# Optimization experiments

Measured on AMD Instinct MI355X. Metric: run time of the kernel, lower is better.

The kernel has to match this reference:

```python
import jax, jax.numpy as jnp
import numpy as np

DIM = 4096
RATIO = 0.5
K = max(1, int(np.ceil(RATIO * DIM)))  # 2048


def setup_inputs() -> dict:
    key = jax.random.key(0)
    x = jax.random.normal(key, (4, 4096, DIM), dtype=jnp.float32)
    return {"x": x}


def reference(x):
    # Eval-mode exact path of TopKSiLU with _thr == 0:
    #   h = silu(x); thr = kth largest |h| per row; zero entries with |h| < thr.
    h = jax.nn.silu(x)
    abs_h = jnp.abs(h)
    # torch kthvalue(dim - k + 1) over ascending order == k-th largest value.
    topk_vals, _ = jax.lax.top_k(abs_h, K)          # [..., K], descending
    thr = topk_vals[..., -1:]                        # [..., 1] per-row threshold
    return jnp.where(abs_h < thr, jnp.zeros((), x.dtype), h)
```

## Files before the change

kernel.cpp:

```cpp
#include <hip/hip_runtime.h>
#include <math.h>

#define DIM      4096
#define KSEL     2048
#define NTHREADS 256
#define VPT      16
#define NREP     8
#define HSTRIDE  257
#define HREP_SZ  (NREP * HSTRIDE)

__device__ __forceinline__ float cephes_expf_fma(float x) {
    const float LOG2EF = 1.44269504088896341f;
    const float C1     = 0.693359375f;
    const float C2     = -2.12194440e-4f;
    float z0 = __builtin_fmaf(x, LOG2EF, 0.5f);
    float fx = floorf(z0);
    float r  = __fsub_rn(x, __fmul_rn(fx, C1));
    r = __builtin_fmaf(fx, -C2, r);
    float zz = __fmul_rn(r, r);
    float y  = 1.9875691500e-4f;
    y = __builtin_fmaf(y, r, 1.3981999507e-3f);
    y = __builtin_fmaf(y, r, 8.3334519073e-3f);
    y = __builtin_fmaf(y, r, 4.1665795894e-2f);
    y = __builtin_fmaf(y, r, 1.6666665459e-1f);
    y = __builtin_fmaf(y, r, 5.0000001201e-1f);
    y = __builtin_fmaf(y, zz, r);
    y = __fadd_rn(y, 1.0f);
    int n = (int)fx;
    float scale = __int_as_float((n + 127) << 23);
    return __fmul_rn(y, scale);
}

__device__ __forceinline__ float silu_ref(float x) {
    float e = cephes_expf_fma(-x);
    float s = __fdiv_rn(1.0f, __fadd_rn(1.0f, e));
    return __fmul_rn(x, s);
}

__global__ __launch_bounds__(NTHREADS) void topk_silu_kernel(
    const float* __restrict__ x, float* __restrict__ out)
{
    const int row  = blockIdx.x;
    const int tid  = threadIdx.x;
    const int lane = tid & 63;
    const int wave = tid >> 6;

    const float4* __restrict__ xr4 =
        reinterpret_cast<const float4*>(x + (size_t)row * DIM);
    float4* __restrict__ or4 =
        reinterpret_cast<float4*>(out + (size_t)row * DIM);

    __shared__ int      hrep[HREP_SZ];
    __shared__ int      hist1[256];
    __shared__ int      wtot[4];
    __shared__ unsigned s_dig;
    __shared__ int      s_krem;

    float    hv[VPT];
    unsigned ub[VPT];
    #pragma unroll
    for (int j = 0; j < 4; ++j) {
        float4 v = xr4[j * NTHREADS + tid];
        const float* vp = &v.x;
        #pragma unroll
        for (int c4 = 0; c4 < 4; ++c4) {
            float h = silu_ref(vp[c4]);
            hv[j*4+c4] = h;
            ub[j*4+c4] = __float_as_uint(h) & 0x7FFFFFFFu;
        }
    }

    #pragma unroll
    for (int i = 0; i < (HREP_SZ + NTHREADS - 1) / NTHREADS; ++i) {
        int idx = tid + i * NTHREADS;
        if (idx < HREP_SZ) hrep[idx] = 0;
    }
    hist1[tid] = 0;
    __syncthreads();

    const int rep = tid & (NREP - 1);
    #pragma unroll
    for (int r = 0; r < VPT; ++r)
        atomicAdd(&hrep[rep * HSTRIDE + (ub[r] >> 24)], 1);
    __syncthreads();

    int c = 0;
    #pragma unroll
    for (int g = 0; g < NREP; ++g)
        c += hrep[g * HSTRIDE + tid];

    int s = c;
    #pragma unroll
    for (int off = 1; off < 64; off <<= 1) {
        int t = __shfl_down(s, off);
        if (lane + off < 64) s += t;
    }
    if (lane == 0) wtot[wave] = s;
    __syncthreads();
    #pragma unroll
    for (int w = 0; w < 4; ++w)
        if (w > wave) s += wtot[w];

    int krem = KSEL;
    if (s >= krem && s - c < krem) {
        s_dig  = (unsigned)tid;
        s_krem = krem - (s - c);
    }
    __syncthreads();
    unsigned prefix = s_dig << 24;
    krem = s_krem;

    #pragma unroll 1
    for (int pass = 1; pass < 4; ++pass) {
        const int shift = 24 - pass * 8;
        const unsigned himask = 0xFFFFFFFFu << (shift + 8);

        #pragma unroll
        for (int r = 0; r < VPT; ++r) {
            unsigned b = ub[r];
            if ((b & himask) == prefix)
                atomicAdd(&hist1[(b >> shift) & 255u], 1);
        }
        __syncthreads();

        c = hist1[tid];
        s = c;
        #pragma unroll
        for (int off = 1; off < 64; off <<= 1) {
            int t = __shfl_down(s, off);
            if (lane + off < 64) s += t;
        }
        if (lane == 0) wtot[wave] = s;
        __syncthreads();
        #pragma unroll
        for (int w = 0; w < 4; ++w)
            if (w > wave) s += wtot[w];

        if (s >= krem && s - c < krem) {
            s_dig  = (unsigned)tid;
            s_krem = krem - (s - c);
        }
        hist1[tid] = 0;
        __syncthreads();
        prefix |= s_dig << shift;
        krem    = s_krem;
    }

    const unsigned tb = prefix;
    #pragma unroll
    for (int j = 0; j < 4; ++j) {
        float4 o;
        o.x = (ub[j*4+0] >= tb) ? hv[j*4+0] : 0.0f;
        o.y = (ub[j*4+1] >= tb) ? hv[j*4+1] : 0.0f;
        o.z = (ub[j*4+2] >= tb) ? hv[j*4+2] : 0.0f;
        o.w = (ub[j*4+3] >= tb) ? hv[j*4+3] : 0.0f;
        or4[j * NTHREADS + tid] = o;
    }
}

extern "C" void kernel_launch(void* const* d_in, const int* in_sizes, int n_in,
                              void* d_out, int out_size, void* d_ws, size_t ws_size,
                              hipStream_t stream) {
    const float* x   = (const float*)d_in[0];
    float*       out = (float*)d_out;
    const int rows = in_sizes[0] / DIM;
    topk_silu_kernel<<<rows, NTHREADS, 0, stream>>>(x, out);
}
```

Baseline: 114.9 us.

## Process two rows per block to amortize radix-select barriers and latency

Each block now handles two rows at once, running both radix-select histograms, scans and passes interleaved, so every barrier and shuffle round serves two rows. It also stops keeping separate float and masked-bits arrays and stores only the raw bits, recomputing the abs mask when needed to cut register use. The goal is more independent work per wave to hide memory and sync latency. The trade-offs are doubled shared memory per block, higher register pressure and half as many blocks, which may lower occupancy, and the launch assumes an even row count.

Result: slower. 118.7 us (+3.3%).

```diff
diff --git a/kernel.cpp b/kernel.cpp
--- a/kernel.cpp
+++ b/kernel.cpp
@@ -40,75 +40,78 @@
 __global__ __launch_bounds__(NTHREADS) void topk_silu_kernel(
     const float* __restrict__ x, float* __restrict__ out)
 {
-    const int row  = blockIdx.x;
     const int tid  = threadIdx.x;
     const int lane = tid & 63;
     const int wave = tid >> 6;
+    const int rep  = tid & (NREP - 1);
 
-    const float4* __restrict__ xr4 =
-        reinterpret_cast<const float4*>(x + (size_t)row * DIM);
-    float4* __restrict__ or4 =
-        reinterpret_cast<float4*>(out + (size_t)row * DIM);
+    const size_t rowA = (size_t)blockIdx.x * 2;
+    const float4* __restrict__ xa = reinterpret_cast<const float4*>(x + rowA * DIM);
+    const float4* __restrict__ xb = reinterpret_cast<const float4*>(x + (rowA + 1) * DIM);
+    float4* __restrict__ oa = reinterpret_cast<float4*>(out + rowA * DIM);
+    float4* __restrict__ ob = reinterpret_cast<float4*>(out + (rowA + 1) * DIM);
 
-    __shared__ int      hrep[HREP_SZ];
-    __shared__ int      hist1[256];
-    __shared__ int      wtot[4];
-    __shared__ unsigned s_dig;
-    __shared__ int      s_krem;
+    __shared__ int      hrep[2][HREP_SZ];
+    __shared__ int      hist1[2][256];
+    __shared__ int      wtot[2][4];
+    __shared__ unsigned s_dig[2];
+    __shared__ int      s_krem[2];
 
-    float    hv[VPT];
-    unsigned ub[VPT];
+    unsigned hbA[VPT], hbB[VPT];
     #pragma unroll
     for (int j = 0; j < 4; ++j) {
-        float4 v = xr4[j * NTHREADS + tid];
-        const float* vp = &v.x;
+        float4 va = xa[j * NTHREADS + tid];
+        float4 vb = xb[j * NTHREADS + tid];
+        const float* ap = &va.x;
+        const float* bp = &vb.x;
         #pragma unroll
         for (int c4 = 0; c4 < 4; ++c4) {
-            float h = silu_ref(vp[c4]);
-            hv[j*4+c4] = h;
-            ub[j*4+c4] = __float_as_uint(h) & 0x7FFFFFFFu;
+            hbA[j*4+c4] = __float_as_uint(silu_ref(ap[c4]));
+            hbB[j*4+c4] = __float_as_uint(silu_ref(bp[c4]));
         }
     }
 
     #pragma unroll
-    for (int i = 0; i < (HREP_SZ + NTHREADS - 1) / NTHREADS; ++i) {
+    for (int i = 0; i < (2 * HREP_SZ + NTHREADS - 1) / NTHREADS; ++i) {
         int idx = tid + i * NTHREADS;
-        if (idx < HREP_SZ) hrep[idx] = 0;
+        if (idx < 2 * HREP_SZ) (&hrep[0][0])[idx] = 0;
     }
-    hist1[tid] = 0;
+    hist1[0][tid] = 0;
+    hist1[1][tid] = 0;
     __syncthreads();
 
-    const int rep = tid & (NREP - 1);
     #pragma unroll
-    for (int r = 0; r < VPT; ++r)
-        atomicAdd(&hrep[rep * HSTRIDE + (ub[r] >> 24)], 1);
+    for (int r = 0; r < VPT; ++r) {
+        atomicAdd(&hrep[0][rep * HSTRIDE + ((hbA[r] & 0x7FFFFFFFu) >> 24)], 1);
+        atomicAdd(&hrep[1][rep * HSTRIDE + ((hbB[r] & 0x7FFFFFFFu) >> 24)], 1);
+    }
     __syncthreads();
 
-    int c = 0;
+    int cA = 0, cB = 0;
     #pragma unroll
-    for (int g = 0; g < NREP; ++g)
-        c += hrep[g * HSTRIDE + tid];
+    for (int g = 0; g < NREP; ++g) {
+        cA += hrep[0][g * HSTRIDE + tid];
+        cB += hrep[1][g * HSTRIDE + tid];
+    }
 
-    int s = c;
+    int sA = cA, sB = cB;
     #pragma unroll
     for (int off = 1; off < 64; off <<= 1) {
-        int t = __shfl_down(s, off);
-        if (lane + off < 64) s += t;
+        int tA = __shfl_down(sA, off);
+        int tB = __shfl_down(sB, off);
+        if (lane + off < 64) { sA += tA; sB += tB; }
     }
-    if (lane == 0) wtot[wave] = s;
+    if (lane == 0) { wtot[0][wave] = sA; wtot[1][wave] = sB; }
     __syncthreads();
     #pragma unroll
     for (int w = 0; w < 4; ++w)
-        if (w > wave) s += wtot[w];
+        if (w > wave) { sA += wtot[0][w]; sB += wtot[1][w]; }
 
-    int krem = KSEL;
-    if (s >= krem && s - c < krem) {
-        s_dig  = (unsigned)tid;
-        s_krem = krem - (s - c);
-    }
+    if (sA >= KSEL && sA - cA < KSEL) { s_dig[0] = (unsigned)tid; s_krem[0] = KSEL - (sA - cA); }
+    if (sB >= KSEL && sB - cB < KSEL) { s_dig[1] = (unsigned)tid; s_krem[1] = KSEL - (sB - cB); }
     __syncthreads();
-    unsigned prefix = s_dig << 24;
-    krem = s_krem;
+    unsigned prefA = s_dig[0] << 24, prefB = s_dig[1] << 24;
+    int      kremA = s_krem[0],      kremB = s_krem[1];
 
     #pragma unroll 1
     for (int pass = 1; pass < 4; ++pass) {
@@ -117,44 +120,49 @@
 
         #pragma unroll
         for (int r = 0; r < VPT; ++r) {
-            unsigned b = ub[r];
-            if ((b & himask) == prefix)
-                atomicAdd(&hist1[(b >> shift) & 255u], 1);
+            unsigned bA = hbA[r] & 0x7FFFFFFFu;
+            unsigned bB = hbB[r] & 0x7FFFFFFFu;
+            if ((bA & himask) == prefA) atomicAdd(&hist1[0][(bA >> shift) & 255u], 1);
+            if ((bB & himask) == prefB) atomicAdd(&hist1[1][(bB >> shift) & 255u], 1);
         }
         __syncthreads();
 
-        c = hist1[tid];
-        s = c;
+        cA = hist1[0][tid]; cB = hist1[1][tid];
+        sA = cA; sB = cB;
         #pragma unroll
         for (int off = 1; off < 64; off <<= 1) {
-            int t = __shfl_down(s, off);
-            if (lane + off < 64) s += t;
+            int tA = __shfl_down(sA, off);
+            int tB = __shfl_down(sB, off);
+            if (lane + off < 64) { sA += tA; sB += tB; }
         }
-        if (lane == 0) wtot[wave] = s;
+        if (lane == 0) { wtot[0][wave] = sA; wtot[1][wave] = sB; }
         __syncthreads();
         #pragma unroll
         for (int w = 0; w < 4; ++w)
-            if (w > wave) s += wtot[w];
+            if (w > wave) { sA += wtot[0][w]; sB += wtot[1][w]; }
 
-        if (s >= krem && s - c < krem) {
-            s_dig  = (unsigned)tid;
-            s_krem = krem - (s - c);
-        }
-        hist1[tid] = 0;
+        if (sA >= kremA && sA - cA < kremA) { s_dig[0] = (unsigned)tid; s_krem[0] = kremA - (sA - cA); }
+        if (sB >= kremB && sB - cB < kremB) { s_dig[1] = (unsigned)tid; s_krem[1] = kremB - (sB - cB); }
+        hist1[0][tid] = 0;
+        hist1[1][tid] = 0;
         __syncthreads();
-        prefix |= s_dig << shift;
-        krem    = s_krem;
+        prefA |= s_dig[0] << shift;  kremA = s_krem[0];
+        prefB |= s_dig[1] << shift;  kremB = s_krem[1];
     }
 
-    const unsigned tb = prefix;
     #pragma unroll
     for (int j = 0; j < 4; ++j) {
-        float4 o;
-        o.x = (ub[j*4+0] >= tb) ? hv[j*4+0] : 0.0f;
-        o.y = (ub[j*4+1] >= tb) ? hv[j*4+1] : 0.0f;
-        o.z = (ub[j*4+2] >= tb) ? hv[j*4+2] : 0.0f;
-        o.w = (ub[j*4+3] >= tb) ? hv[j*4+3] : 0.0f;
-        or4[j * NTHREADS + tid] = o;
+        float4 oA, oB;
+        float* pa = &oA.x;
+        float* pb = &oB.x;
+        #pragma unroll
+        for (int c4 = 0; c4 < 4; ++c4) {
+            unsigned ha = hbA[j*4+c4], hb = hbB[j*4+c4];
+            pa[c4] = ((ha & 0x7FFFFFFFu) >= prefA) ? __uint_as_float(ha) : 0.0f;
+            pb[c4] = ((hb & 0x7FFFFFFFu) >= prefB) ? __uint_as_float(hb) : 0.0f;
+        }
+        oa[j * NTHREADS + tid] = oA;
+        ob[j * NTHREADS + tid] = oB;
     }
 }
 
@@ -164,5 +172,5 @@
     const float* x   = (const float*)d_in[0];
     float*       out = (float*)d_out;
     const int rows = in_sizes[0] / DIM;
-    topk_silu_kernel<<<rows, NTHREADS, 0, stream>>>(x, out);
+    topk_silu_kernel<<<rows / 2, NTHREADS, 0, stream>>>(x, out);
 }
```
